# Kernel optimization log

Measured on AMD Instinct MI355X. Metric: run time of the kernel, lower is better.

## Reference

```python
import jax, jax.numpy as jnp
import numpy as np

EPS = 1e-5   # torch nn.LayerNorm default
H = 12       # num_heads


def layernorm(x, w, b):
    m = jnp.mean(x, axis=-1, keepdims=True)
    v = jnp.var(x, axis=-1, keepdims=True)
    return (x - m) * jax.lax.rsqrt(v + EPS) * w + b


def mha(x, qkv_w, proj_w, proj_b):
    # MemEffAttention math (qkv_bias=False, proj_bias=True), block-diagonal mask
    # over equal-length sequences == independent per-row attention.
    B, N, D = x.shape
    hd = D // H
    qkv = jnp.einsum('bnd,ed->bne', x, qkv_w).reshape(B, N, 3, H, hd)
    q, k, v = qkv[:, :, 0], qkv[:, :, 1], qkv[:, :, 2]
    scale = hd ** -0.5
    attn = jnp.einsum('bnhd,bmhd->bhnm', q * scale, k)     # [B,H,N,N]
    attn = jax.nn.softmax(attn, axis=-1)
    o = jnp.einsum('bhnm,bmhd->bnhd', attn, v).reshape(B, N, D)
    return jnp.einsum('bnd,ed->bne', o, proj_w) + proj_b


def block(x, ln1_w, ln1_b, qkv_w, proj_w, proj_b, ln2_w, ln2_b, fc1_w, fc1_b, fc2_w, fc2_b):
    # x = x + attn(norm1(x)); x = x + mlp(norm2(x))  (ls1/ls2 = Identity, eval mode)
    x = x + mha(layernorm(x, ln1_w, ln1_b), qkv_w, proj_w, proj_b)
    h = layernorm(x, ln2_w, ln2_b)
    h = jax.nn.gelu(jnp.einsum('bnd,ed->bne', h, fc1_w) + fc1_b, approximate=False)
    h = jnp.einsum('bne,de->bnd', h, fc2_w) + fc2_b
    return x + h


def setup_inputs() -> dict:
    key = jax.random.key(0)
    ks = jax.random.split(key, 8)
    D, Dff = 768, 3072
    s = lambda k, shape, sc: jax.random.normal(k, shape, jnp.float32) * sc
    return {
        'x1': s(ks[0], (8, 1370, D), 1.0),
        'x2': s(ks[1], (8, 257, D), 1.0),
        'ln1_w': jnp.ones((D,), jnp.float32), 'ln1_b': jnp.zeros((D,), jnp.float32),
        'qkv_w': s(ks[2], (3 * D, D), 0.02),
        'proj_w': s(ks[3], (D, D), 0.02), 'proj_b': jnp.zeros((D,), jnp.float32),
        'ln2_w': jnp.ones((D,), jnp.float32), 'ln2_b': jnp.zeros((D,), jnp.float32),
        'fc1_w': s(ks[4], (Dff, D), 0.02), 'fc1_b': jnp.zeros((Dff,), jnp.float32),
        'fc2_w': s(ks[5], (D, Dff), 0.02), 'fc2_b': jnp.zeros((D,), jnp.float32),
    }


def reference(x1, x2, ln1_w, ln1_b, qkv_w, proj_w, proj_b, ln2_w, ln2_b,
              fc1_w, fc1_b, fc2_w, fc2_b):
    # forward_nested (eval path): block-diagonal attention over nested groups,
    # which factorizes into per-group batched attention; return the
    # concatenated token stream (same values as attn_bias.split output).
    params = (ln1_w, ln1_b, qkv_w, proj_w, proj_b, ln2_w, ln2_b,
              fc1_w, fc1_b, fc2_w, fc2_b)
    o1 = block(x1, *params)
    o2 = block(x2, *params)
    D = x1.shape[-1]
    return jnp.concatenate([o1.reshape(-1, D), o2.reshape(-1, D)], axis=0)
```

## Files before the change

### kernel.cpp

```cpp
#include <hip/hip_runtime.h>
#include <hip/hip_bf16.h>

typedef __attribute__((ext_vector_type(8))) short bf16x8;
typedef __attribute__((ext_vector_type(4))) float f32x4;
typedef __attribute__((ext_vector_type(16))) float f32x16;

#define GL_LDS16(g, l)                                                        \
  __builtin_amdgcn_global_load_lds((const __attribute__((address_space(1))) void*)(g), \
                                   (__attribute__((address_space(3))) void*)(l), 16, 0, 0)

__device__ __forceinline__ ushort f2bf(float f) {
  union { float f; unsigned u; } x; x.f = f;
  unsigned r = x.u + 0x7fffu + ((x.u >> 16) & 1u);
  return (ushort)(r >> 16);
}

__device__ __forceinline__ int xcd_remap(int bid, int nwg) {
  int q = nwg >> 3, r = nwg & 7;
  int xcd = bid & 7, idx = bid >> 3;
  return (xcd < r ? xcd * (q + 1) : r * (q + 1) + (xcd - r) * q) + idx;
}

__global__ void cvt_kernel(const float* __restrict__ in, ushort* __restrict__ out, int n) {
  int i = blockIdx.x * blockDim.x + threadIdx.x;
  int stride = gridDim.x * blockDim.x;
  for (; i < n; i += stride) out[i] = f2bf(in[i]);
}

__global__ __launch_bounds__(64) void ln_kernel(
    const float* __restrict__ x1, const float* __restrict__ x2, int M1,
    const float* __restrict__ w, const float* __restrict__ b,
    ushort* __restrict__ out) {
  int row = blockIdx.x;
  int lane = threadIdx.x;
  const float* xr = (row < M1) ? x1 + (size_t)row * 768
                               : x2 + (size_t)(row - M1) * 768;
  float4 v[3];
  float s = 0.f, sq = 0.f;
#pragma unroll
  for (int i = 0; i < 3; i++) {
    v[i] = *(const float4*)(xr + i * 256 + lane * 4);
    s += v[i].x + v[i].y + v[i].z + v[i].w;
    sq += v[i].x * v[i].x + v[i].y * v[i].y + v[i].z * v[i].z + v[i].w * v[i].w;
  }
#pragma unroll
  for (int m = 1; m < 64; m <<= 1) { s += __shfl_xor(s, m); sq += __shfl_xor(sq, m); }
  float mean = s * (1.f / 768.f);
  float var = sq * (1.f / 768.f) - mean * mean;
  float rstd = rsqrtf(var + 1e-5f);
  ushort* orow = out + (size_t)row * 768;
#pragma unroll
  for (int i = 0; i < 3; i++) {
    int d = i * 256 + lane * 4;
    float4 wv = *(const float4*)(w + d);
    float4 bv = *(const float4*)(b + d);
    ushort4 o;
    o.x = f2bf((v[i].x - mean) * rstd * wv.x + bv.x);
    o.y = f2bf((v[i].y - mean) * rstd * wv.y + bv.y);
    o.z = f2bf((v[i].z - mean) * rstd * wv.z + bv.z);
    o.w = f2bf((v[i].w - mean) * rstd * wv.w + bv.w);
    *(ushort4*)(orow + d) = o;
  }
}

template <int MODE>
__global__ __launch_bounds__(256) void gemm_tile(
    const ushort* __restrict__ A, const ushort* __restrict__ W,
    const float* __restrict__ bias, void* __restrict__ outp,
    int M, int N, int K, int ncol) {
  __shared__ ushort lA[128 * 64];
  __shared__ ushort lB[128 * 64];
  const int t = threadIdx.x;
  const int lane = t & 63, wave = t >> 6;
  const int l15 = lane & 15, lg = lane >> 4;
  const int waveM = wave >> 1, waveN = wave & 1;
  const int g = xcd_remap(blockIdx.x, gridDim.x);
  const int rowBlk = (g / ncol) * 128;
  const int colBlk = (g % ncol) * 128;
  const int srow = t >> 3;
  const int schunk = t & 7;

  f32x4 acc[4][4] = {};

  for (int k0 = 0; k0 < K; k0 += 64) {
    if (k0) __syncthreads();
#pragma unroll
    for (int i = 0; i < 4; i++) {
      int row = i * 32 + srow;
      int gch = schunk ^ (row & 7);
      GL_LDS16(A + (size_t)(rowBlk + row) * K + k0 + gch * 8,
               &lA[row * 64 + schunk * 8]);
      GL_LDS16(W + (size_t)(colBlk + row) * K + k0 + gch * 8,
               &lB[row * 64 + schunk * 8]);
    }
    __syncthreads();
#pragma unroll
    for (int kk = 0; kk < 2; kk++) {
      bf16x8 af[4], bfr[4];
#pragma unroll
      for (int m = 0; m < 4; m++) {
        int row = waveM * 64 + m * 16 + l15;
        af[m] = *(const bf16x8*)&lA[row * 64 + ((kk * 32 + lg * 8) ^ ((row & 7) << 3))];
      }
#pragma unroll
      for (int c = 0; c < 4; c++) {
        int row = waveN * 64 + c * 16 + l15;
        bfr[c] = *(const bf16x8*)&lB[row * 64 + ((kk * 32 + lg * 8) ^ ((row & 7) << 3))];
      }
#pragma unroll
      for (int m = 0; m < 4; m++)
#pragma unroll
        for (int c = 0; c < 4; c++)
          acc[m][c] = __builtin_amdgcn_mfma_f32_16x16x32_bf16(af[m], bfr[c], acc[m][c], 0, 0, 0);
    }
  }

  const float qsc = (MODE == 0 && colBlk < 768) ? 0.18033688011112042f : 1.f;
#pragma unroll
  for (int m = 0; m < 4; m++) {
    int rowB = rowBlk + waveM * 64 + m * 16 + lg * 4;
#pragma unroll
    for (int c = 0; c < 4; c++) {
      int col = colBlk + waveN * 64 + c * 16 + l15;
      float bv = (MODE == 2) ? bias[col] : 0.f;
#pragma unroll
      for (int j = 0; j < 4; j++) {
        int r = rowB + j;
        if (r < M) {
          float v = acc[m][c][j] + bv;
          size_t idx = (size_t)r * N + col;
          if (MODE == 2) {
            float gl = 0.5f * v * (1.f + erff(v * 0.70710678118f));
            ((ushort*)outp)[idx] = f2bf(gl);
          } else {
            ((ushort*)outp)[idx] = f2bf(v * qsc);
          }
        }
      }
    }
  }
}

__global__ __launch_bounds__(256) void gemm_tile64(
    const ushort* __restrict__ A, const ushort* __restrict__ W,
    const float* __restrict__ bias, const float* __restrict__ res1,
    const float* __restrict__ res2, int resSplit,
    float* __restrict__ outp, int M, int N, int K, int ncol) {
  __shared__ ushort lA[64 * 64];
  __shared__ ushort lB[128 * 64];
  const int t = threadIdx.x;
  const int lane = t & 63, wave = t >> 6;
  const int l15 = lane & 15, lg = lane >> 4;
  const int waveM = wave >> 1, waveN = wave & 1;
  const int g = xcd_remap(blockIdx.x, gridDim.x);
  const int rowBlk = (g / ncol) * 64;
  const int colBlk = (g % ncol) * 128;
  const int srow = t >> 3;
  const int schunk = t & 7;

  f32x4 acc[2][4] = {};

  for (int k0 = 0; k0 < K; k0 += 64) {
    if (k0) __syncthreads();
#pragma unroll
    for (int i = 0; i < 2; i++) {
      int row = i * 32 + srow;
      int gch = schunk ^ (row & 7);
      GL_LDS16(A + (size_t)(rowBlk + row) * K + k0 + gch * 8,
               &lA[row * 64 + schunk * 8]);
    }
#pragma unroll
    for (int i = 0; i < 4; i++) {
      int row = i * 32 + srow;
      int gch = schunk ^ (row & 7);
      GL_LDS16(W + (size_t)(colBlk + row) * K + k0 + gch * 8,
               &lB[row * 64 + schunk * 8]);
    }
    __syncthreads();
#pragma unroll
    for (int kk = 0; kk < 2; kk++) {
      bf16x8 af[2], bfr[4];
#pragma unroll
      for (int m = 0; m < 2; m++) {
        int row = waveM * 32 + m * 16 + l15;
        af[m] = *(const bf16x8*)&lA[row * 64 + ((kk * 32 + lg * 8) ^ ((row & 7) << 3))];
      }
#pragma unroll
      for (int c = 0; c < 4; c++) {
        int row = waveN * 64 + c * 16 + l15;
        bfr[c] = *(const bf16x8*)&lB[row * 64 + ((kk * 32 + lg * 8) ^ ((row & 7) << 3))];
      }
#pragma unroll
      for (int m = 0; m < 2; m++)
#pragma unroll
        for (int c = 0; c < 4; c++)
          acc[m][c] = __builtin_amdgcn_mfma_f32_16x16x32_bf16(af[m], bfr[c], acc[m][c], 0, 0, 0);
    }
  }

#pragma unroll
  for (int m = 0; m < 2; m++) {
    int rowB = rowBlk + waveM * 32 + m * 16 + lg * 4;
#pragma unroll
    for (int c = 0; c < 4; c++) {
      int col = colBlk + waveN * 64 + c * 16 + l15;
      float bv = bias[col];
#pragma unroll
      for (int j = 0; j < 4; j++) {
        int r = rowB + j;
        if (r < M) {
          size_t idx = (size_t)r * N + col;
          float rv = (r < resSplit) ? res1[idx]
                                    : res2[(size_t)(r - resSplit) * N + col];
          outp[idx] = acc[m][c][j] + bv + rv;
        }
      }
    }
  }
}

__global__ __launch_bounds__(256) void prep_kernel(
    const ushort* __restrict__ qkv, ushort* __restrict__ kt2,
    ushort* __restrict__ vt2, int N1, int N2, int nkv1, int nkv2, int M1) {
  __shared__ ushort lT[64 * 68];
  const int t = threadIdx.x;
  const int kv = blockIdx.x;
  const int bhg = blockIdx.y;
  const int part = bhg >= 96;
  const int bh = part ? bhg - 96 : bhg;
  const int N = part ? N2 : N1;
  const int nkv = part ? nkv2 : nkv1;
  if (kv >= nkv) return;
  const size_t rowbase = part ? (size_t)M1 : 0;
  const int b = bh / 12, h = bh % 12;
  const int k0 = kv * 64;
  const ushort* Kp = qkv + (rowbase + (size_t)b * N) * 2304 + 768 + h * 64;
  const ushort* Vp = Kp + 768;
  size_t tbase = (part ? (size_t)96 * nkv1 : 0) + (size_t)bh * nkv + kv;
  ushort* ktile = kt2 + tbase * 4096;
  ushort* vtile = vt2 + tbase * 4096;
#pragma unroll
  for (int p = 0; p < 2; p++) {
    int s = p * 256 + t;
    int chunk = s >> 6, krow = s & 63;
    ushort4 v0 = {0, 0, 0, 0}, v1 = {0, 0, 0, 0};
    if (k0 + krow < N) {
      const ushort* src = Kp + (size_t)(k0 + krow) * 2304 + chunk * 8;
      v0 = *(const ushort4*)src;
      v1 = *(const ushort4*)(src + 4);
    }
    *(ushort4*)&ktile[s * 8] = v0;
    *(ushort4*)&ktile[s * 8 + 4] = v1;
  }
#pragma unroll
  for (int p = 0; p < 2; p++) {
    int nl = p * 32 + (t >> 3);
    int dc = t & 7;
    ushort4 v0 = {0, 0, 0, 0}, v1 = {0, 0, 0, 0};
    if (k0 + nl < N) {
      const ushort* src = Vp + (size_t)(k0 + nl) * 2304 + dc * 8;
      v0 = *(const ushort4*)src;
      v1 = *(const ushort4*)(src + 4);
    }
    *(ushort4*)&lT[nl * 68 + dc * 8] = v0;
    *(ushort4*)&lT[nl * 68 + dc * 8 + 4] = v1;
  }
  __syncthreads();
#pragma unroll
  for (int p = 0; p < 2; p++) {
    int s = p * 256 + t;
    int kchunk = s >> 6, d = s & 63;
    ushort o[8];
#pragma unroll
    for (int j = 0; j < 8; j++) o[j] = lT[(kchunk * 8 + j) * 68 + d];
    *(ushort4*)&vtile[s * 8] = *(ushort4*)o;
    *(ushort4*)&vtile[s * 8 + 4] = *(ushort4*)(o + 4);
  }
}

#define ATTN_STAGE(buf, kvi)                                                   \
  do {                                                                         \
    _Pragma("unroll") for (int p = 0; p < 2; p++) {                            \
      int s = p * 256 + t;                                                     \
      GL_LDS16(tK + (size_t)(kvi) * 4096 + s * 8, &lK[buf][s * 8]);            \
      GL_LDS16(tV + (size_t)(kvi) * 4096 + s * 8, &lV[buf][s * 8]);            \
    }                                                                          \
  } while (0)

__global__ __launch_bounds__(256) void attn_kernel(
    const ushort* __restrict__ qkv, const ushort* __restrict__ kt2,
    const ushort* __restrict__ vt2, ushort* __restrict__ o_out,
    int N1, int N2, int nkv1, int nkv2, int M1) {
  __shared__ ushort lK[2][4096];
  __shared__ ushort lV[2][4096];
  const int t = threadIdx.x;
  const int lane = t & 63, wave = t >> 6;
  const int l31 = lane & 31, hi = lane >> 5;
  const int bhg = blockIdx.y;
  const int part = bhg >= 96;
  const int bh = part ? bhg - 96 : bhg;
  const int N = part ? N2 : N1;
  const int nkv = part ? nkv2 : nkv1;
  const int qb = blockIdx.x * 128;
  if (qb >= N) return;
  const size_t rowbase = part ? (size_t)M1 : 0;
  const int b = bh / 12, h = bh % 12;
  const ushort* Qp = qkv + (rowbase + (size_t)b * N) * 2304 + h * 64;
  const size_t tboff = (part ? (size_t)96 * nkv1 : 0) + (size_t)bh * nkv;
  const ushort* tK = kt2 + tboff * 4096;
  const ushort* tV = vt2 + tboff * 4096;

  const int qrow = qb + wave * 32 + l31;
  bf16x8 qf[4];
#pragma unroll
  for (int kc = 0; kc < 4; kc++)
    qf[kc] = *(const bf16x8*)(Qp + (size_t)qrow * 2304 + kc * 16 + hi * 8);

  f32x16 oacc[2] = {};
  float mrun = -1e30f, lrun = 0.f;

  ATTN_STAGE(0, 0);
  __syncthreads();
  for (int kv = 0; kv < nkv; kv++) {
    int cur = kv & 1;
    if (kv + 1 < nkv) ATTN_STAGE(cur ^ 1, kv + 1);
    const bool fullTile = (kv * 64 + 64 <= N);
    f32x16 sacc0 = {}, sacc1 = {};
#pragma unroll
    for (int kc = 0; kc < 4; kc++) {
      bf16x8 kf0 = *(const bf16x8*)&lK[cur][(((kc * 2 + hi) << 6) + l31) * 8];
      bf16x8 kf1 = *(const bf16x8*)&lK[cur][(((kc * 2 + hi) << 6) + 32 + l31) * 8];
      sacc0 = __builtin_amdgcn_mfma_f32_32x32x16_bf16(kf0, qf[kc], sacc0, 0, 0, 0);
      sacc1 = __builtin_amdgcn_mfma_f32_32x32x16_bf16(kf1, qf[kc], sacc1, 0, 0, 0);
    }
    float z[32];
#pragma unroll
    for (int r = 0; r < 16; r++) { z[r] = sacc0[r]; z[16 + r] = sacc1[r]; }
    if (!fullTile) {
#pragma unroll
      for (int i = 0; i < 32; i++) {
        int kg = kv * 64 + (i >> 4) * 32 + (i & 3) + (((i & 15) >> 2) << 3) + (hi << 2);
        if (kg >= N) z[i] = -1e30f;
      }
    }
    float m16[16], m8[8], m4[4], m2[2];
#pragma unroll
    for (int i = 0; i < 16; i++) m16[i] = fmaxf(z[i], z[i + 16]);
#pragma unroll
    for (int i = 0; i < 8; i++) m8[i] = fmaxf(m16[i], m16[i + 8]);
#pragma unroll
    for (int i = 0; i < 4; i++) m4[i] = fmaxf(m8[i], m8[i + 4]);
    m2[0] = fmaxf(m4[0], m4[2]); m2[1] = fmaxf(m4[1], m4[3]);
    float mx = fmaxf(m2[0], m2[1]);
    {
      float a = mx, bx = mx;
      asm("v_permlane32_swap_b32 %0, %1" : "+&v"(a), "+v"(bx));
      mx = fmaxf(a, bx);
    }
    if (!__all(mx <= mrun + 8.f)) {
      float mnew = fmaxf(mrun, mx);
      float corr = exp2f(mrun - mnew);
      lrun *= corr;
      oacc[0] *= corr;
      oacc[1] *= corr;
      mrun = mnew;
    }
#pragma unroll
    for (int i = 0; i < 32; i++) z[i] = exp2f(z[i] - mrun);
    float s16[16], s8[8], s4[4];
#pragma unroll
    for (int i = 0; i < 16; i++) s16[i] = z[i] + z[i + 16];
#pragma unroll
    for (int i = 0; i < 8; i++) s8[i] = s16[i] + s16[i + 8];
#pragma unroll
    for (int i = 0; i < 4; i++) s4[i] = s8[i] + s8[i + 4];
    float rs = (s4[0] + s4[1]) + (s4[2] + s4[3]);
    {
      float a = rs, bx = rs;
      asm("v_permlane32_swap_b32 %0, %1" : "+&v"(a), "+v"(bx));
      rs = a + bx;
    }
    lrun += rs;
#pragma unroll
    for (int kt = 0; kt < 2; kt++) {
      unsigned w0[4], w1[4];
#pragma unroll
      for (int rr = 0; rr < 4; rr++) {
        asm("v_cvt_pk_bf16_f32 %0, %1, %2" : "=v"(w0[rr]) : "v"(z[kt * 16 + 4 * rr]), "v"(z[kt * 16 + 4 * rr + 1]));
        asm("v_cvt_pk_bf16_f32 %0, %1, %2" : "=v"(w1[rr]) : "v"(z[kt * 16 + 4 * rr + 2]), "v"(z[kt * 16 + 4 * rr + 3]));
      }
#pragma unroll
      for (int kc2 = 0; kc2 < 2; kc2++) {
        unsigned ua = w0[2 * kc2], ub = w0[2 * kc2 + 1];
        unsigned uc = w1[2 * kc2], ud = w1[2 * kc2 + 1];
        asm("v_permlane32_swap_b32 %0, %1" : "+&v"(ua), "+v"(ub));
        asm("v_permlane32_swap_b32 %0, %1" : "+&v"(uc), "+v"(ud));
        union { unsigned u[4]; bf16x8 v; } pa;
        pa.u[0] = ua; pa.u[1] = uc; pa.u[2] = ub; pa.u[3] = ud;
        int kcg = kt * 2 + kc2;
#pragma unroll
        for (int dt = 0; dt < 2; dt++) {
          bf16x8 vf = *(const bf16x8*)&lV[cur][(((kcg * 2 + hi) << 6) + dt * 32 + l31) * 8];
          oacc[dt] = __builtin_amdgcn_mfma_f32_32x32x16_bf16(pa.v, vf, oacc[dt], 0, 0, 0);
        }
      }
    }
    __syncthreads();
  }
  float inv = 1.f / lrun;
#pragma unroll
  for (int dt = 0; dt < 2; dt++)
#pragma unroll
    for (int r = 0; r < 16; r++) {
      int q = qb + wave * 32 + (r & 3) + ((r >> 2) << 3) + (hi << 2);
      if (q < N)
        o_out[(rowbase + (size_t)b * N + q) * 768 + h * 64 + dt * 32 + l31] =
            f2bf(oacc[dt][r] * inv);
    }
}

extern "C" void kernel_launch(void* const* d_in, const int* in_sizes, int n_in,
                              void* d_out, int out_size, void* d_ws, size_t ws_size,
                              hipStream_t stream) {
  const float* x1 = (const float*)d_in[0];
  const float* x2 = (const float*)d_in[1];
  const float* ln1_w = (const float*)d_in[2];
  const float* ln1_b = (const float*)d_in[3];
  const float* qkv_w = (const float*)d_in[4];
  const float* proj_w = (const float*)d_in[5];
  const float* proj_b = (const float*)d_in[6];
  const float* ln2_w = (const float*)d_in[7];
  const float* ln2_b = (const float*)d_in[8];
  const float* fc1_w = (const float*)d_in[9];
  const float* fc1_b = (const float*)d_in[10];
  const float* fc2_w = (const float*)d_in[11];
  const float* fc2_b = (const float*)d_in[12];
  float* out = (float*)d_out;

  const int N1 = 1370, N2 = 257;
  const int M1 = 8 * N1, M2 = 8 * N2;
  const int MT = M1 + M2;
  const int MPAD = 13056;
  const int nkv1 = 22, nkv2 = 5;

  char* ws = (char*)d_ws;
  ushort* wq = (ushort*)ws;   ws += (size_t)2304 * 768 * 2;
  ushort* wp = (ushort*)ws;   ws += (size_t)768 * 768 * 2;
  ushort* w1 = (ushort*)ws;   ws += (size_t)3072 * 768 * 2;
  ushort* w2 = (ushort*)ws;   ws += (size_t)768 * 3072 * 2;
  ushort* bufA = (ushort*)ws;   ws += (size_t)MPAD * 768 * 2;
  ushort* bufQKV = (ushort*)ws; ws += (size_t)MPAD * 2304 * 2;
  ushort* bufFF = (ushort*)ws;  ws += (size_t)MPAD * 3072 * 2;
  const size_t nTiles = (size_t)96 * (nkv1 + nkv2);
  ushort* kt2 = bufFF;
  ushort* vt2 = bufFF + nTiles * 4096;

  cvt_kernel<<<2048, 256, 0, stream>>>(qkv_w, wq, 2304 * 768);
  cvt_kernel<<<2048, 256, 0, stream>>>(proj_w, wp, 768 * 768);
  cvt_kernel<<<2048, 256, 0, stream>>>(fc1_w, w1, 3072 * 768);
  cvt_kernel<<<2048, 256, 0, stream>>>(fc2_w, w2, 768 * 3072);

  ln_kernel<<<MT, 64, 0, stream>>>(x1, x2, M1, ln1_w, ln1_b, bufA);
  gemm_tile<0><<<(MPAD / 128) * 18, 256, 0, stream>>>(
      bufA, wq, nullptr, bufQKV, MT, 2304, 768, 18);
  prep_kernel<<<dim3(nkv1, 192), 256, 0, stream>>>(bufQKV, kt2, vt2, N1, N2, nkv1, nkv2, M1);
  attn_kernel<<<dim3((N1 + 127) / 128, 192), 256, 0, stream>>>(
      bufQKV, kt2, vt2, bufA, N1, N2, nkv1, nkv2, M1);
  gemm_tile64<<<(MPAD / 64) * 6, 256, 0, stream>>>(
      bufA, wp, proj_b, x1, x2, M1, out, MT, 768, 768, 6);
  ln_kernel<<<MT, 64, 0, stream>>>(out, out, MT, ln2_w, ln2_b, bufA);
  gemm_tile<2><<<(MPAD / 128) * 24, 256, 0, stream>>>(
      bufA, w1, fc1_b, bufFF, MT, 3072, 768, 24);
  gemm_tile64<<<(MPAD / 64) * 6, 256, 0, stream>>>(
      bufFF, w2, fc2_b, out, nullptr, MT, out, MT, 768, 3072, 6);
}
```

Before: 484.9 us.

## Compute softmax denominator via MFMA, add setprio around MFMAs, max3 reductions

The attention kernel now gets the softmax row sum from an extra MFMA that multiplies P by a ones vector, which removes the scalar add-tree and cross-lane swap. The row max reduction uses v_max3 and the normalisation uses v_rcp. s_setprio is raised around the MFMA blocks in both GEMMs and in attention to favour the waves issuing matrix instructions. Query rows are clamped to avoid out-of-range loads, and the attention grid is hardcoded to 11 blocks, which matches ceil(1370/128) for this shape only. In exchange each KV step issues one extra MFMA, and the sum accumulates bf16-rounded probabilities.

After: 488.3 us. No clear change (+0.7%).

```diff
diff --git a/kernel.cpp b/kernel.cpp
--- a/kernel.cpp
+++ b/kernel.cpp
@@ -13,6 +13,12 @@
   union { float f; unsigned u; } x; x.f = f;
   unsigned r = x.u + 0x7fffu + ((x.u >> 16) & 1u);
   return (ushort)(r >> 16);
+}
+
+__device__ __forceinline__ float max3f(float a, float b, float c) {
+  float d;
+  asm("v_max3_f32 %0, %1, %2, %3" : "=v"(d) : "v"(a), "v"(b), "v"(c));
+  return d;
 }
 
 __device__ __forceinline__ int xcd_remap(int bid, int nwg) {
@@ -107,11 +113,13 @@
         int row = waveN * 64 + c * 16 + l15;
         bfr[c] = *(const bf16x8*)&lB[row * 64 + ((kk * 32 + lg * 8) ^ ((row & 7) << 3))];
       }
+      __builtin_amdgcn_s_setprio(1);
 #pragma unroll
       for (int m = 0; m < 4; m++)
 #pragma unroll
         for (int c = 0; c < 4; c++)
           acc[m][c] = __builtin_amdgcn_mfma_f32_16x16x32_bf16(af[m], bfr[c], acc[m][c], 0, 0, 0);
+      __builtin_amdgcn_s_setprio(0);
     }
   }
 
@@ -190,11 +198,13 @@
         int row = waveN * 64 + c * 16 + l15;
         bfr[c] = *(const bf16x8*)&lB[row * 64 + ((kk * 32 + lg * 8) ^ ((row & 7) << 3))];
       }
+      __builtin_amdgcn_s_setprio(1);
 #pragma unroll
       for (int m = 0; m < 2; m++)
 #pragma unroll
         for (int c = 0; c < 4; c++)
           acc[m][c] = __builtin_amdgcn_mfma_f32_16x16x32_bf16(af[m], bfr[c], acc[m][c], 0, 0, 0);
+      __builtin_amdgcn_s_setprio(0);
     }
   }
 
@@ -310,14 +320,19 @@
   const ushort* tK = kt2 + tboff * 4096;
   const ushort* tV = vt2 + tboff * 4096;
 
-  const int qrow = qb + wave * 32 + l31;
+  const int qrow = min(qb + wave * 32 + l31, N - 1);
   bf16x8 qf[4];
 #pragma unroll
   for (int kc = 0; kc < 4; kc++)
     qf[kc] = *(const bf16x8*)(Qp + (size_t)qrow * 2304 + kc * 16 + hi * 8);
 
+  union { unsigned u[4]; bf16x8 v; } ones;
+#pragma unroll
+  for (int i = 0; i < 4; i++) ones.u[i] = 0x3F803F80u;
+
   f32x16 oacc[2] = {};
-  float mrun = -1e30f, lrun = 0.f;
+  f32x16 osum = {};
+  float mrun = -1e30f;
 
   ATTN_STAGE(0, 0);
   __syncthreads();
@@ -326,6 +341,7 @@
     if (kv + 1 < nkv) ATTN_STAGE(cur ^ 1, kv + 1);
     const bool fullTile = (kv * 64 + 64 <= N);
     f32x16 sacc0 = {}, sacc1 = {};
+    __builtin_amdgcn_s_setprio(1);
 #pragma unroll
     for (int kc = 0; kc < 4; kc++) {
       bf16x8 kf0 = *(const bf16x8*)&lK[cur][(((kc * 2 + hi) << 6) + l31) * 8];
@@ -333,6 +349,7 @@
       sacc0 = __builtin_amdgcn_mfma_f32_32x32x16_bf16(kf0, qf[kc], sacc0, 0, 0, 0);
       sacc1 = __builtin_amdgcn_mfma_f32_32x32x16_bf16(kf1, qf[kc], sacc1, 0, 0, 0);
     }
+    __builtin_amdgcn_s_setprio(0);
     float z[32];
 #pragma unroll
     for (int r = 0; r < 16; r++) { z[r] = sacc0[r]; z[16 + r] = sacc1[r]; }
@@ -343,15 +360,15 @@
         if (kg >= N) z[i] = -1e30f;
       }
     }
-    float m16[16], m8[8], m4[4], m2[2];
-#pragma unroll
-    for (int i = 0; i < 16; i++) m16[i] = fmaxf(z[i], z[i + 16]);
-#pragma unroll
-    for (int i = 0; i < 8; i++) m8[i] = fmaxf(m16[i], m16[i + 8]);
-#pragma unroll
-    for (int i = 0; i < 4; i++) m4[i] = fmaxf(m8[i], m8[i + 4]);
-    m2[0] = fmaxf(m4[0], m4[2]); m2[1] = fmaxf(m4[1], m4[3]);
-    float mx = fmaxf(m2[0], m2[1]);
+    float mA[11];
+#pragma unroll
+    for (int i = 0; i < 10; i++) mA[i] = max3f(z[3 * i], z[3 * i + 1], z[3 * i + 2]);
+    mA[10] = fmaxf(z[30], z[31]);
+    float mB[4];
+#pragma unroll
+    for (int i = 0; i < 3; i++) mB[i] = max3f(mA[3 * i], mA[3 * i + 1], mA[3 * i + 2]);
+    mB[3] = fmaxf(mA[9], mA[10]);
+    float mx = fmaxf(max3f(mB[0], mB[1], mB[2]), mB[3]);
     {
       float a = mx, bx = mx;
       asm("v_permlane32_swap_b32 %0, %1" : "+&v"(a), "+v"(bx));
@@ -360,27 +377,13 @@
     if (!__all(mx <= mrun + 8.f)) {
       float mnew = fmaxf(mrun, mx);
       float corr = exp2f(mrun - mnew);
-      lrun *= corr;
       oacc[0] *= corr;
       oacc[1] *= corr;
+      osum *= corr;
       mrun = mnew;
     }
 #pragma unroll
     for (int i = 0; i < 32; i++) z[i] = exp2f(z[i] - mrun);
-    float s16[16], s8[8], s4[4];
-#pragma unroll
-    for (int i = 0; i < 16; i++) s16[i] = z[i] + z[i + 16];
-#pragma unroll
-    for (int i = 0; i < 8; i++) s8[i] = s16[i] + s16[i + 8];
-#pragma unroll
-    for (int i = 0; i < 4; i++) s4[i] = s8[i] + s8[i + 4];
-    float rs = (s4[0] + s4[1]) + (s4[2] + s4[3]);
-    {
-      float a = rs, bx = rs;
-      asm("v_permlane32_swap_b32 %0, %1" : "+&v"(a), "+v"(bx));
-      rs = a + bx;
-    }
-    lrun += rs;
 #pragma unroll
     for (int kt = 0; kt < 2; kt++) {
       unsigned w0[4], w1[4];
@@ -398,25 +401,29 @@
         union { unsigned u[4]; bf16x8 v; } pa;
         pa.u[0] = ua; pa.u[1] = uc; pa.u[2] = ub; pa.u[3] = ud;
         int kcg = kt * 2 + kc2;
+        __builtin_amdgcn_s_setprio(1);
 #pragma unroll
         for (int dt = 0; dt < 2; dt++) {
           bf16x8 vf = *(const bf16x8*)&lV[cur][(((kcg * 2 + hi) << 6) + dt * 32 + l31) * 8];
           oacc[dt] = __builtin_amdgcn_mfma_f32_32x32x16_bf16(pa.v, vf, oacc[dt], 0, 0, 0);
         }
+        osum = __builtin_amdgcn_mfma_f32_32x32x16_bf16(pa.v, ones.v, osum, 0, 0, 0);
+        __builtin_amdgcn_s_setprio(0);
       }
     }
     __syncthreads();
   }
-  float inv = 1.f / lrun;
-#pragma unroll
-  for (int dt = 0; dt < 2; dt++)
-#pragma unroll
-    for (int r = 0; r < 16; r++) {
-      int q = qb + wave * 32 + (r & 3) + ((r >> 2) << 3) + (hi << 2);
-      if (q < N)
-        o_out[(rowbase + (size_t)b * N + q) * 768 + h * 64 + dt * 32 + l31] =
-            f2bf(oacc[dt][r] * inv);
-    }
+#pragma unroll
+  for (int r = 0; r < 16; r++) {
+    int q = qb + wave * 32 + (r & 3) + ((r >> 2) << 3) + (hi << 2);
+    if (q < N) {
+      float inv;
+      asm("v_rcp_f32 %0, %1" : "=v"(inv) : "v"(osum[r]));
+      ushort* orow = o_out + (rowbase + (size_t)b * N + q) * 768 + h * 64;
+      orow[l31] = f2bf(oacc[0][r] * inv);
+      orow[32 + l31] = f2bf(oacc[1][r] * inv);
+    }
+  }
 }
 
 extern "C" void kernel_launch(void* const* d_in, const int* in_sizes, int n_in,
@@ -464,7 +471,7 @@
   gemm_tile<0><<<(MPAD / 128) * 18, 256, 0, stream>>>(
       bufA, wq, nullptr, bufQKV, MT, 2304, 768, 18);
   prep_kernel<<<dim3(nkv1, 192), 256, 0, stream>>>(bufQKV, kt2, vt2, N1, N2, nkv1, nkv2, M1);
-  attn_kernel<<<dim3((N1 + 127) / 128, 192), 256, 0, stream>>>(
+  attn_kernel<<<dim3(11, 192), 256, 0, stream>>>(
       bufQKV, kt2, vt2, bufA, N1, N2, nkv1, nkv2, M1);
   gemm_tile64<<<(MPAD / 64) * 6, 256, 0, stream>>>(
       bufA, wp, proj_b, x1, x2, M1, out, MT, 768, 768, 6);
```
